# Kernel optimization log

Hardware: AMD Instinct MI355X
Metric: run time of the kernel (lower is better)

Reference implementation:

```python
import jax, jax.numpy as jnp
import numpy as np

E = 2.718281828459045  # math.e
B, A, N = 128, 512, 256


def setup_inputs() -> dict:
    key = jax.random.key(0)
    k1, k2, k3 = jax.random.split(key, 3)
    # atomic numbers: positive integers (1..89) stored as float32
    atomic_numbers = jax.random.randint(k1, (B, A), 1, 90).astype(jnp.float32)
    # neighbor indices into the atom axis [0, A)
    neighbors = jax.random.randint(k2, (B, A, N), 0, A).astype(jnp.int32)
    # pairwise distances, positive
    r_ij = jax.random.uniform(k3, (B, A, N), dtype=jnp.float32) * 5.0 + 0.5
    return {"atomic_numbers": atomic_numbers, "neighbors": neighbors, "r_ij": r_ij}


def reference(atomic_numbers, neighbors, r_ij):
    # a_i: [B, A, 1] central-atom atomic numbers
    a_i = atomic_numbers[:, :, None]
    # gather neighbor atomic numbers: out[b,i,j] = atomic_numbers[b, neighbors[b,i,j]]
    a_j = jax.vmap(lambda an, nb: an[nb])(atomic_numbers, neighbors)  # [B, A, N]
    # fused elementwise edit: exp(-0.05*e * (a_i*a_j)^1.01 / (a_i+a_j)^1.1)
    dist_edit = jnp.exp(-0.05 * E * jnp.power(a_i * a_j, 1.01)
                        / jnp.power(a_i + a_j, 1.1))
    return r_ij + dist_edit
```

## Files before the change

### kernel.cpp

```cpp
#include <hip/hip_runtime.h>


#define BB 128
#define AA 512
#define NN 256
#define ROWS 32
#define TPB 256
#define TABN 8192

typedef int   v4i __attribute__((ext_vector_type(4)));
typedef float v4f __attribute__((ext_vector_type(4)));

__device__ __forceinline__ float tab_entry(int idx) {
    int zi = idx / 90, zj = idx - zi * 90;
    float p = fmaxf((float)(zi * zj), 1.0f);
    float s = fmaxf((float)(zi + zj), 1.0f);
    const float c = -0.05f * 2.718281828459045f;
    return __expf(c * __powf(p, 1.01f) / __powf(s, 1.1f));
}

__global__ void RAN_72567767433723_build_tab(_Float16* __restrict__ tabg) {
    int idx = blockIdx.x * blockDim.x + threadIdx.x;
    tabg[idx] = (_Float16)tab_entry(idx);
}

template <bool LOAD_TAB>
__global__ __launch_bounds__(TPB, 4) void RAN_72567767433723_kernel(
    const float* __restrict__ an,
    const int*   __restrict__ nbrs,
    const float* __restrict__ rij,
    float*       __restrict__ out,
    const _Float16* __restrict__ tabg)
{
    __shared__ _Float16       tab[TABN];
    __shared__ unsigned short zz[AA];

    const int tid      = threadIdx.x;
    const int b        = blockIdx.x >> 4;
    const int row_base = (blockIdx.x & 15) * ROWS;

    if (LOAD_TAB) {
        #pragma unroll
        for (int i = 0; i < TABN * 2 / (16 * TPB); ++i) {
            int k = i * TPB + tid;
            ((v4i*)tab)[k] = ((const v4i*)tabg)[k];
        }
    } else {
        for (int idx = tid; idx < TABN; idx += TPB)
            tab[idx] = (_Float16)tab_entry(idx);
    }
    #pragma unroll
    for (int i = tid; i < AA; i += TPB)
        zz[i] = (unsigned short)(int)(an[b * AA + i] + 0.5f);
    __syncthreads();

    const int w  = tid >> 6;
    const int l  = tid & 63;
    const int a0 = row_base + w;
    const size_t base = ((size_t)(b * AA + a0)) * NN + (size_t)(l * 4);

    v4i nb[8]; v4f rj[8];
    #pragma unroll
    for (int it = 0; it < 8; ++it) {
        const size_t e = base + (size_t)(it * 4) * NN;
        nb[it] = __builtin_nontemporal_load((const v4i*)(nbrs + e));
        rj[it] = __builtin_nontemporal_load((const v4f*)(rij + e));
    }

    int tb[8];
    #pragma unroll
    for (int it = 0; it < 8; ++it)
        tb[it] = (int)zz[a0 + it * 4] * 90;

    #pragma unroll
    for (int it = 0; it < 8; ++it) {
        const size_t e = base + (size_t)(it * 4) * NN;
        v4f o;
        o.x = rj[it].x + (float)tab[tb[it] + (int)zz[nb[it].x]];
        o.y = rj[it].y + (float)tab[tb[it] + (int)zz[nb[it].y]];
        o.z = rj[it].z + (float)tab[tb[it] + (int)zz[nb[it].z]];
        o.w = rj[it].w + (float)tab[tb[it] + (int)zz[nb[it].w]];
        __builtin_nontemporal_store(o, (v4f*)(out + e));
    }
}

extern "C" void kernel_launch(void* const* d_in, const int* in_sizes, int n_in,
                              void* d_out, int out_size, void* d_ws, size_t ws_size,
                              hipStream_t stream) {
    const float* an  = (const float*)d_in[0];
    const int*   nbr = (const int*)d_in[1];
    const float* rij = (const float*)d_in[2];
    float*       o   = (float*)d_out;

    const int grid = (BB * AA) / ROWS;

    if (ws_size >= (size_t)TABN * sizeof(_Float16)) {
        _Float16* tabg = (_Float16*)d_ws;
        RAN_72567767433723_build_tab<<<TABN / TPB, TPB, 0, stream>>>(tabg);
        RAN_72567767433723_kernel<true><<<grid, TPB, 0, stream>>>(an, nbr, rij, o, tabg);
    } else {
        RAN_72567767433723_kernel<false><<<grid, TPB, 0, stream>>>(an, nbr, rij, o, nullptr);
    }
}
```

Before: 166.1 us.

## Drop separate table-build kernel; compute table in-block overlapped with streaming loads

Removes the separate kernel that wrote the fp16 lookup table to workspace. Each block now issues its global loads for neighbors, r_ij and atomic numbers first, then computes the 8192-entry table in shared memory while those loads are in flight. This saves one launch and its global round-trip, but every one of the 2048 blocks now evaluates 32 exp/pow entries per thread, which adds transcendental work to each block.

```diff
diff --git a/kernel.cpp b/kernel.cpp
--- a/kernel.cpp
+++ b/kernel.cpp
@@ -19,18 +19,11 @@
     return __expf(c * __powf(p, 1.01f) / __powf(s, 1.1f));
 }
 
-__global__ void RAN_72567767433723_build_tab(_Float16* __restrict__ tabg) {
-    int idx = blockIdx.x * blockDim.x + threadIdx.x;
-    tabg[idx] = (_Float16)tab_entry(idx);
-}
-
-template <bool LOAD_TAB>
 __global__ __launch_bounds__(TPB, 4) void RAN_72567767433723_kernel(
     const float* __restrict__ an,
     const int*   __restrict__ nbrs,
     const float* __restrict__ rij,
-    float*       __restrict__ out,
-    const _Float16* __restrict__ tabg)
+    float*       __restrict__ out)
 {
     __shared__ _Float16       tab[TABN];
     __shared__ unsigned short zz[AA];
@@ -39,25 +32,15 @@
     const int b        = blockIdx.x >> 4;
     const int row_base = (blockIdx.x & 15) * ROWS;
 
-    if (LOAD_TAB) {
-        #pragma unroll
-        for (int i = 0; i < TABN * 2 / (16 * TPB); ++i) {
-            int k = i * TPB + tid;
-            ((v4i*)tab)[k] = ((const v4i*)tabg)[k];
-        }
-    } else {
-        for (int idx = tid; idx < TABN; idx += TPB)
-            tab[idx] = (_Float16)tab_entry(idx);
-    }
-    #pragma unroll
-    for (int i = tid; i < AA; i += TPB)
-        zz[i] = (unsigned short)(int)(an[b * AA + i] + 0.5f);
-    __syncthreads();
-
     const int w  = tid >> 6;
     const int l  = tid & 63;
     const int a0 = row_base + w;
     const size_t base = ((size_t)(b * AA + a0)) * NN + (size_t)(l * 4);
+
+    float anv[AA / TPB];
+    #pragma unroll
+    for (int i = 0; i < AA / TPB; ++i)
+        anv[i] = an[b * AA + i * TPB + tid];
 
     v4i nb[8]; v4f rj[8];
     #pragma unroll
@@ -66,6 +49,16 @@
         nb[it] = __builtin_nontemporal_load((const v4i*)(nbrs + e));
         rj[it] = __builtin_nontemporal_load((const v4f*)(rij + e));
     }
+
+    #pragma unroll 4
+    for (int i = 0; i < TABN / TPB; ++i) {
+        int idx = i * TPB + tid;
+        tab[idx] = (_Float16)tab_entry(idx);
+    }
+    #pragma unroll
+    for (int i = 0; i < AA / TPB; ++i)
+        zz[i * TPB + tid] = (unsigned short)(int)(anv[i] + 0.5f);
+    __syncthreads();
 
     int tb[8];
     #pragma unroll
@@ -93,12 +86,5 @@
     float*       o   = (float*)d_out;
 
     const int grid = (BB * AA) / ROWS;
-
-    if (ws_size >= (size_t)TABN * sizeof(_Float16)) {
-        _Float16* tabg = (_Float16*)d_ws;
-        RAN_72567767433723_build_tab<<<TABN / TPB, TPB, 0, stream>>>(tabg);
-        RAN_72567767433723_kernel<true><<<grid, TPB, 0, stream>>>(an, nbr, rij, o, tabg);
-    } else {
-        RAN_72567767433723_kernel<false><<<grid, TPB, 0, stream>>>(an, nbr, rij, o, nullptr);
-    }
+    RAN_72567767433723_kernel<<<grid, TPB, 0, stream>>>(an, nbr, rij, o);
 }
```

New measurement: 265.0 us. 1.6x slower.
